# Performance work log

Measured on AMD Instinct MI355X. Metric: run time of the kernel, lower is better.

Reference implementation:

```python
import jax, jax.numpy as jnp
import numpy as np

NUM_HEADS = 16
NUM_GQA_GROUPS = 4
HEAD_DIM = 128
TOTAL_TOKENS = 4096
NUM_SEQS = 8
SCALE = HEAD_DIM ** -0.5


def setup_inputs() -> dict:
    key = jax.random.key(0)
    kq, kk, kv, kc = jax.random.split(key, 4)
    query = jax.random.normal(kq, (TOTAL_TOKENS, NUM_HEADS, HEAD_DIM), dtype=jnp.float32)
    k = jax.random.normal(kk, (TOTAL_TOKENS, NUM_GQA_GROUPS, HEAD_DIM), dtype=jnp.float32)
    v = jax.random.normal(kv, (TOTAL_TOKENS, NUM_GQA_GROUPS, HEAD_DIM), dtype=jnp.float32)
    # cu_seqlens: sorted prefix boundaries, pinned to 0 and TOTAL_TOKENS
    inner = jnp.sort(jax.random.randint(kc, (NUM_SEQS - 1,), 1, TOTAL_TOKENS, dtype=jnp.int32))
    cu_seqlens = jnp.concatenate([
        jnp.zeros((1,), jnp.int32), inner,
        jnp.full((1,), TOTAL_TOKENS, jnp.int32)])
    return {"query": query, "key": k, "value": v, "cu_seqlens": cu_seqlens}


def reference(query, key, value, cu_seqlens):
    """Packed varlen (thd) causal attention with GQA, fused via a segment mask.

    query: [T, H, D]; key/value: [T, G, D]; cu_seqlens: [B+1] int32.
    Returns [T, H, D] (same layout the torch thd path concatenates back to).
    """
    T, H, D = query.shape
    ratio = H // key.shape[1]
    if ratio > 1:  # GQA: repeat kv heads to match query heads
        key = jnp.repeat(key, ratio, axis=1)
        value = jnp.repeat(value, ratio, axis=1)

    pos = jnp.arange(T, dtype=jnp.int32)
    # segment id of each packed token: cu[j] <= i < cu[j+1]
    seg = jnp.searchsorted(cu_seqlens, pos, side="right") - 1
    # within-segment causal mask (global causal == local causal inside a segment)
    mask = (seg[:, None] == seg[None, :]) & (pos[:, None] >= pos[None, :])  # [T, T]

    scores = jnp.einsum("qhd,khd->hqk", query, key) * SCALE  # [H, T, T]
    scores = jnp.where(mask[None], scores, -jnp.inf)
    probs = jax.nn.softmax(scores, axis=-1)
    out = jnp.einsum("hqk,khd->qhd", probs, value)  # [T, H, D]
    return out
```

## Files before the change

kernel.cpp:

```cpp
#include <hip/hip_runtime.h>
#include <hip/hip_bf16.h>


#define T_TOK 4096
#define NH    16
#define NG    4
#define HD    128
#define NCU   9
#define NTILE 128

#define ML_OFF  33554432l
#define Q_OFF   34603008l
#define KBF_OFF 34607620l
#define VTB_OFF 35656196l
#define WS_END  36704772l

typedef short          short8_t __attribute__((ext_vector_type(8)));
typedef float          float4_t __attribute__((ext_vector_type(4)));
typedef unsigned int   uint2_t  __attribute__((ext_vector_type(2)));
typedef unsigned short ushort;

static __device__ inline unsigned pack2(float a, float b) {
    __hip_bfloat162 h = __float22bfloat162_rn(make_float2(a, b));
    union { __hip_bfloat162 h; unsigned u; } c; c.h = h;
    return c.u;
}
static __device__ inline short8_t cvt8(float4_t lo, float4_t hi) {
    union { unsigned u[4]; short8_t s; } r;
    r.u[0] = pack2(lo[0], lo[1]); r.u[1] = pack2(lo[2], lo[3]);
    r.u[2] = pack2(hi[0], hi[1]); r.u[3] = pack2(hi[2], hi[3]);
    return r.s;
}
static __device__ inline float bf2f(ushort u) {
    union { unsigned i; float f; } c; c.i = ((unsigned)u) << 16; return c.f;
}
static __device__ __forceinline__ void chunk_geom(int nblk, int& chunk, int& nce) {
    int nc0 = (nblk + 11) / 12;
    if (nc0 > 8) nc0 = 8;
    chunk = (((nblk + nc0 - 1) / nc0) + 1) & ~1;
    nce   = (nblk + chunk - 1) / chunk;
}

#define NPK 1048576l
__global__ __launch_bounds__(256) void prep_all(
    const float* __restrict__ K, const float* __restrict__ V,
    const int* __restrict__ cu, float* __restrict__ WS)
{
    const int b = (int)blockIdx.x, tid = (int)threadIdx.x;
    if (b < 512) {
        unsigned* Kb = (unsigned*)(WS + KBF_OFF);
        for (long p = (long)b * 256 + tid; p < NPK; p += 512l * 256) {
            const float2 v = *(const float2*)&K[2 * p];
            Kb[p] = pack2(v.x, v.y);
        }
    } else if (b < 1536) {
        ushort* Vtb = (ushort*)(WS + VTB_OFF);
        const int bt  = b - 512;
        const int g   = bt >> 8;
        const int rem = bt & 255;
        const int d0  = (rem >> 6) * 32;
        const int t0  = (rem & 63) * 64;
        __shared__ ushort tile[64][36];
        const int i2 = tid >> 3, jl = (tid & 7) * 4;
        #pragma unroll
        for (int ii = 0; ii < 2; ++ii) {
            const int t = t0 + i2 + ii * 32;
            const float4_t v = *(const float4_t*)&V[((long)t * NG + g) * HD + d0 + jl];
            *(unsigned*)&tile[i2 + ii * 32][jl]     = pack2(v[0], v[1]);
            *(unsigned*)&tile[i2 + ii * 32][jl + 2] = pack2(v[2], v[3]);
        }
        __syncthreads();
        const int jj = tid >> 3, tl = (tid & 7) * 8;
        union { ushort s[8]; short8_t v; } o;
        #pragma unroll
        for (int r = 0; r < 8; ++r) o.s[r] = tile[tl + r][jj];
        *(short8_t*)&Vtb[((long)(g * HD + d0 + jj)) * T_TOK + t0 + tl] = o.v;
    } else {
        int* qwork = (int*)(WS + Q_OFF);
        __shared__ int nblk_s[NTILE];
        __shared__ int sortedE[NTILE + 1];
        if (tid >= 128) return;
        const int t = tid;
        const int qbase = t * 32;
        int seg0 = 0;
        #pragma unroll
        for (int j = 1; j < NCU; ++j) { int cj = cu[j]; if (cj <= qbase) seg0 = cj; }
        const int k0   = seg0 & ~31;
        const int nblk = (qbase + 32 - k0) >> 5;
        nblk_s[t] = nblk;
        __syncthreads();
        int r = 0;
        for (int j = 0; j < NTILE; ++j) {
            int nj = nblk_s[j];
            if (nj > nblk || (nj == nblk && j < t)) ++r;
        }
        int chunk, nce; chunk_geom(nblk, chunk, nce);
        sortedE[r] = 4 * nce;
        __syncthreads();
        if (t == 0) {
            int s = 0;
            for (int j = 0; j < NTILE; ++j) { int v = sortedE[j]; sortedE[j] = s; s += v; }
            sortedE[NTILE] = s;
            qwork[0] = s;
            qwork[1] = 0;
        }
        __syncthreads();
        int off = 2 + sortedE[r];
        for (int g = 0; g < NG; ++g)
            for (int cz = 0; cz < nce; ++cz)
                qwork[off++] = (t << 5) | (g << 3) | cz;
    }
}

template <bool CHB>
static __device__ __forceinline__ void attn_tile_body(
    const float* __restrict__ Q, const float* __restrict__ K,
    const float* __restrict__ V,
    const ushort* __restrict__ Kb, const ushort* __restrict__ Vtb,
    const int* __restrict__ cu,
    float* __restrict__ O, float* __restrict__ WS,
    unsigned char* smem, int qtile, int g, int cz)
{
    ushort (*Ks)[32][136]   = (ushort (*)[32][136])smem;
    ushort (*Vt)[128][40]   = (ushort (*)[128][40])(smem + 17408);
    ushort (*pb)[2][16][40] = (ushort (*)[2][16][40])(smem + 37888);

    const int tid   = threadIdx.x;
    const int wave  = tid >> 6;
    const int split = wave >> 2;
    const int hw    = wave & 3;
    const int lane  = tid & 63;
    const int h     = g * 4 + hw;
    const int col   = lane & 15;
    const int quad  = lane >> 4;

    const int qbase = qtile * 32;
    const int qq[2] = { qbase + col, qbase + 16 + col };

    int seg_start[2] = {0, 0}, seg0 = 0;
    #pragma unroll
    for (int j = 1; j < NCU; ++j) {
        int cj = cu[j];
        if (cj <= qq[0])  seg_start[0] = cj;
        if (cj <= qq[1])  seg_start[1] = cj;
        if (cj <= qbase)  seg0         = cj;
    }
    const int k0       = seg0 & ~31;
    const int nblk_tot = (qbase + 32 - k0) >> 5;

    int nc = 1, kb_lo = 0, nblk = nblk_tot;
    if (CHB) {
        int chunk; chunk_geom(nblk_tot, chunk, nc);
        if (cz >= nc) return;
        kb_lo = cz * chunk;
        nblk  = nblk_tot - kb_lo;
        if (nblk > chunk) nblk = chunk;
    }
    const int nb0    = (nblk + 1) >> 1;
    const int kstart = k0 + (kb_lo + split * nb0) * 32;

    const int smax[2] = { __shfl(seg_start[0], 15), __shfl(seg_start[1], 15) };

    short8_t qf[2][4];
    #pragma unroll
    for (int tt = 0; tt < 2; ++tt) {
        const float* qp = Q + ((long)qq[tt] * NH + h) * HD + quad * 8;
        #pragma unroll
        for (int c = 0; c < 4; ++c)
            qf[tt][c] = cvt8(*(const float4_t*)(qp + c * 32),
                             *(const float4_t*)(qp + c * 32 + 4));
    }

    float4_t oacc[2][8];
    #pragma unroll
    for (int tt = 0; tt < 2; ++tt)
        #pragma unroll
        for (int dt = 0; dt < 8; ++dt) oacc[tt][dt] = (float4_t){0.f, 0.f, 0.f, 0.f};

    float m_run[2] = {-10000.0f, -10000.0f};
    float l_run[2] = {0.0f, 0.0f};
    const float c_scale = 0.08838834764831845f * 1.4426950408889634f;

    const int stid = tid & 255;
    const int ki  = stid >> 3;
    const int ch  = (stid & 7) * 16;
    const int kp2 = (stid & 15) * 2;
    const int dc  = (stid >> 4) * 8;
    const int vd  = stid >> 1;
    const int vko = (stid & 1) * 16;

    float4_t kreg[4], vreg[4];
    short8_t krb[2], vrb[2];
    if constexpr (CHB) {
        int key = kstart + ki; if (key > T_TOK - 1) key = T_TOK - 1;
        const ushort* kp = Kb + ((long)key * NG + g) * HD + ch;
        krb[0] = *(const short8_t*)kp; krb[1] = *(const short8_t*)(kp + 8);
        int ts = kstart + vko; if (ts > T_TOK - 16) ts = T_TOK - 16;
        const ushort* vp = Vtb + ((long)(g * HD + vd)) * T_TOK + ts;
        vrb[0] = *(const short8_t*)vp; vrb[1] = *(const short8_t*)(vp + 8);
    } else {
        int key = kstart + ki; if (key > T_TOK - 1) key = T_TOK - 1;
        const float* kp = K + ((long)key * NG + g) * HD + ch;
        kreg[0] = *(const float4_t*)kp;       kreg[1] = *(const float4_t*)(kp + 4);
        kreg[2] = *(const float4_t*)(kp + 8); kreg[3] = *(const float4_t*)(kp + 12);
        int key0 = kstart + kp2;     if (key0 > T_TOK - 1) key0 = T_TOK - 1;
        int key1 = kstart + kp2 + 1; if (key1 > T_TOK - 1) key1 = T_TOK - 1;
        const float* v0 = V + ((long)key0 * NG + g) * HD + dc;
        const float* v1 = V + ((long)key1 * NG + g) * HD + dc;
        vreg[0] = *(const float4_t*)v0; vreg[1] = *(const float4_t*)(v0 + 4);
        vreg[2] = *(const float4_t*)v1; vreg[3] = *(const float4_t*)(v1 + 4);
    }

    for (int it = 0; it < nb0; ++it) {
        const int kb = kstart + it * 32;
        __syncthreads();

        if constexpr (CHB) {
            *(short8_t*)&Ks[split][ki][ch]      = krb[0];
            *(short8_t*)&Ks[split][ki][ch + 8]  = krb[1];
            *(short8_t*)&Vt[split][vd][vko]     = vrb[0];
            *(short8_t*)&Vt[split][vd][vko + 8] = vrb[1];
        } else {
            *(short8_t*)&Ks[split][ki][ch]     = cvt8(kreg[0], kreg[1]);
            *(short8_t*)&Ks[split][ki][ch + 8] = cvt8(kreg[2], kreg[3]);
            #pragma unroll
            for (int d = 0; d < 4; ++d) {
                *(unsigned*)&Vt[split][dc + d][kp2]     = pack2(vreg[0][d], vreg[2][d]);
                *(unsigned*)&Vt[split][dc + 4 + d][kp2] = pack2(vreg[1][d], vreg[3][d]);
            }
        }
        __syncthreads();

        {
            int nb = kb + 32;
            if constexpr (CHB) {
                int key = nb + ki; if (key > T_TOK - 1) key = T_TOK - 1;
                const ushort* kp = Kb + ((long)key * NG + g) * HD + ch;
                krb[0] = *(const short8_t*)kp; krb[1] = *(const short8_t*)(kp + 8);
                int ts = nb + vko; if (ts > T_TOK - 16) ts = T_TOK - 16;
                const ushort* vp = Vtb + ((long)(g * HD + vd)) * T_TOK + ts;
                vrb[0] = *(const short8_t*)vp; vrb[1] = *(const short8_t*)(vp + 8);
            } else {
                int key = nb + ki; if (key > T_TOK - 1) key = T_TOK - 1;
                const float* kp = K + ((long)key * NG + g) * HD + ch;
                kreg[0] = *(const float4_t*)kp;       kreg[1] = *(const float4_t*)(kp + 4);
                kreg[2] = *(const float4_t*)(kp + 8); kreg[3] = *(const float4_t*)(kp + 12);
                int key0 = nb + kp2;     if (key0 > T_TOK - 1) key0 = T_TOK - 1;
                int key1 = nb + kp2 + 1; if (key1 > T_TOK - 1) key1 = T_TOK - 1;
                const float* v0 = V + ((long)key0 * NG + g) * HD + dc;
                const float* v1 = V + ((long)key1 * NG + g) * HD + dc;
                vreg[0] = *(const float4_t*)v0; vreg[1] = *(const float4_t*)(v0 + 4);
                vreg[2] = *(const float4_t*)v1; vreg[3] = *(const float4_t*)(v1 + 4);
            }
        }

        float4_t st[2][2];
        #pragma unroll
        for (int tt = 0; tt < 2; ++tt)
            #pragma unroll
            for (int t = 0; t < 2; ++t) st[tt][t] = (float4_t){0.f, 0.f, 0.f, 0.f};
        #pragma unroll
        for (int c = 0; c < 4; ++c) {
            short8_t kf0 = *(const short8_t*)&Ks[split][col][c * 32 + quad * 8];
            short8_t kf1 = *(const short8_t*)&Ks[split][16 + col][c * 32 + quad * 8];
            st[0][0] = __builtin_amdgcn_mfma_f32_16x16x32_bf16(kf0, qf[0][c], st[0][0], 0, 0, 0);
            st[0][1] = __builtin_amdgcn_mfma_f32_16x16x32_bf16(kf1, qf[0][c], st[0][1], 0, 0, 0);
            st[1][0] = __builtin_amdgcn_mfma_f32_16x16x32_bf16(kf0, qf[1][c], st[1][0], 0, 0, 0);
            st[1][1] = __builtin_amdgcn_mfma_f32_16x16x32_bf16(kf1, qf[1][c], st[1][1], 0, 0, 0);
        }

        #pragma unroll
        for (int tt = 0; tt < 2; ++tt) {
            float tv[8];
            if (kb + 31 <= qbase + 16 * tt && kb >= smax[tt]) {
                #pragma unroll
                for (int i = 0; i < 8; ++i)
                    tv[i] = st[tt][i >> 2][i & 3] * c_scale;
            } else {
                #pragma unroll
                for (int t = 0; t < 2; ++t)
                    #pragma unroll
                    for (int r = 0; r < 4; ++r) {
                        int key = kb + 16 * t + quad * 4 + r;
                        bool valid = (key <= qq[tt]) && (key >= seg_start[tt]);
                        tv[t * 4 + r] = valid ? st[tt][t][r] * c_scale : -30000.0f;
                    }
            }
            float tmax = tv[0];
            #pragma unroll
            for (int i = 1; i < 8; ++i) tmax = fmaxf(tmax, tv[i]);
            tmax = fmaxf(tmax, __shfl_xor(tmax, 16));
            tmax = fmaxf(tmax, __shfl_xor(tmax, 32));
            const float m_new = fmaxf(m_run[tt], tmax);
            float p[8], ps = 0.f;
            #pragma unroll
            for (int i = 0; i < 8; ++i) { p[i] = __builtin_exp2f(tv[i] - m_new); ps += p[i]; }
            ps += __shfl_xor(ps, 16);
            ps += __shfl_xor(ps, 32);
            if (__any(tmax > m_run[tt])) {
                const float alpha = __builtin_exp2f(m_run[tt] - m_new);
                l_run[tt] = l_run[tt] * alpha + ps;
                m_run[tt] = m_new;
                #pragma unroll
                for (int dt = 0; dt < 8; ++dt) oacc[tt][dt] *= alpha;
            } else {
                l_run[tt] += ps;
            }

            uint2_t w0; w0.x = pack2(p[0], p[1]); w0.y = pack2(p[2], p[3]);
            uint2_t w1; w1.x = pack2(p[4], p[5]); w1.y = pack2(p[6], p[7]);
            *(uint2_t*)&pb[wave][tt][col][quad * 4]      = w0;
            *(uint2_t*)&pb[wave][tt][col][16 + quad * 4] = w1;
        }
        short8_t pf0 = *(const short8_t*)&pb[wave][0][col][quad * 8];
        short8_t pf1 = *(const short8_t*)&pb[wave][1][col][quad * 8];

        #pragma unroll
        for (int dt = 0; dt < 8; ++dt) {
            short8_t vf = *(const short8_t*)&Vt[split][dt * 16 + col][quad * 8];
            oacc[0][dt] = __builtin_amdgcn_mfma_f32_16x16x32_bf16(vf, pf0, oacc[0][dt], 0, 0, 0);
            oacc[1][dt] = __builtin_amdgcn_mfma_f32_16x16x32_bf16(vf, pf1, oacc[1][dt], 0, 0, 0);
        }
    }

    float* Ob = (float*)smem;
    float* cm = (float*)(smem + 34816);
    float* cl = (float*)(smem + 35840);
    #pragma unroll
    for (int tt = 0; tt < 2; ++tt) {
        __syncthreads();
        if (split == 1) {
            if (quad == 0) { cm[hw * 16 + col] = m_run[tt]; cl[hw * 16 + col] = l_run[tt]; }
            float* ob = Ob + (hw * 16 + col) * 132;
            #pragma unroll
            for (int dt = 0; dt < 8; ++dt)
                *(float4_t*)(ob + dt * 16 + quad * 4) = oacc[tt][dt];
        }
        __syncthreads();
        if (split == 0) {
            const float m1 = cm[hw * 16 + col], l1 = cl[hw * 16 + col];
            const float m  = fmaxf(m_run[tt], m1);
            const float a0 = __builtin_exp2f(m_run[tt] - m);
            const float a1 = __builtin_exp2f(m1 - m);
            const float* ob = Ob + (hw * 16 + col) * 132;
            #pragma unroll
            for (int dt = 0; dt < 8; ++dt) {
                float4_t o1 = *(const float4_t*)(ob + dt * 16 + quad * 4);
                oacc[tt][dt] = oacc[tt][dt] * a0 + o1 * a1;
            }
            l_run[tt] = l_run[tt] * a0 + l1 * a1;
            m_run[tt] = m;
        }
    }

    if (split == 0) {
        if (!CHB || nc == 1) {
            #pragma unroll
            for (int tt = 0; tt < 2; ++tt) {
                const float inv_l = 1.0f / l_run[tt];
                float* op = O + ((long)qq[tt] * NH + h) * HD + quad * 4;
                #pragma unroll
                for (int dt = 0; dt < 8; ++dt) {
                    float4_t ov;
                    #pragma unroll
                    for (int r = 0; r < 4; ++r) ov[r] = oacc[tt][dt][r] * inv_l;
                    *(float4_t*)(op + dt * 16) = ov;
                }
            }
        } else {
            const long slot = ((long)(qtile * 4 + g)) * 8 + cz;
            ushort* ob = (ushort*)WS + slot * 16384;
            #pragma unroll
            for (int tt = 0; tt < 2; ++tt) {
                const int row = hw * 32 + tt * 16 + col;
                if (quad == 0) {
                    float* mlp = WS + ML_OFF + slot * 256 + row * 2;
                    mlp[0] = m_run[tt];
                    mlp[1] = l_run[tt];
                }
                ushort* op = ob + row * 128 + quad * 4;
                #pragma unroll
                for (int dt = 0; dt < 8; ++dt) {
                    uint2_t w;
                    w.x = pack2(oacc[tt][dt][0], oacc[tt][dt][1]);
                    w.y = pack2(oacc[tt][dt][2], oacc[tt][dt][3]);
                    *(uint2_t*)(op + dt * 16) = w;
                }
            }
        }
    }
}

__global__ __launch_bounds__(512) void attn_fwd_persist(
    const float* __restrict__ Q,
    const float* __restrict__ K,
    const float* __restrict__ V,
    const int*   __restrict__ cu,
    float*       __restrict__ O,
    float*       __restrict__ WS)
{
    __shared__ __align__(16) unsigned char smem[58368];
    __shared__ int pop_s;
    int* qwork = (int*)(WS + Q_OFF);
    const ushort* Kb  = (const ushort*)(WS + KBF_OFF);
    const ushort* Vtb = (const ushort*)(WS + VTB_OFF);
    const int qtotal = qwork[0];

    for (;;) {
        __syncthreads();
        if (threadIdx.x == 0) pop_s = atomicAdd(&qwork[1], 1);
        __syncthreads();
        const int idx = pop_s;
        if (idx >= qtotal) return;
        const int ent = qwork[2 + idx];
        attn_tile_body<true>(Q, K, V, Kb, Vtb, cu, O, WS, smem,
                             ent >> 5, (ent >> 3) & 3, ent & 7);
    }
}

__global__ __launch_bounds__(512) void attn_fwd_mono(
    const float* __restrict__ Q,
    const float* __restrict__ K,
    const float* __restrict__ V,
    const int*   __restrict__ cu,
    float*       __restrict__ O)
{
    __shared__ __align__(16) unsigned char smem[58368];
    attn_tile_body<false>(Q, K, V, nullptr, nullptr, cu, O, nullptr, smem,
                          (int)gridDim.x - 1 - (int)blockIdx.x,
                          (int)blockIdx.y, 0);
}

__global__ __launch_bounds__(256) void attn_merge(
    const int*   __restrict__ cu,
    const float* __restrict__ WS,
    float*       __restrict__ O)
{
    const int tile  = blockIdx.x;
    const int g     = blockIdx.y;
    const int qbase = tile * 32;
    int seg0 = 0;
    #pragma unroll
    for (int j = 1; j < NCU; ++j) { int cj = cu[j]; if (cj <= qbase) seg0 = cj; }
    const int k0       = seg0 & ~31;
    const int nblk_tot = (qbase + 32 - k0) >> 5;
    int chunk, nc; chunk_geom(nblk_tot, chunk, nc);
    if (nc <= 1) return;

    const int tid  = threadIdx.x;
    const int row  = tid >> 1;
    const int half = tid & 1;
    const int hw   = row >> 5;
    const int q    = row & 31;

    float m = -30000.0f, l = 0.0f;
    float4_t acc[16];
    #pragma unroll
    for (int i = 0; i < 16; ++i) acc[i] = (float4_t){0.f, 0.f, 0.f, 0.f};

    const long sbase = ((long)(tile * 4 + g)) * 8;
    for (int c = 0; c < nc; ++c) {
        const float* mlp = WS + ML_OFF + (sbase + c) * 256 + row * 2;
        const float mc = mlp[0], lc = mlp[1];
        const float mn = fmaxf(m, mc);
        const float a0 = __builtin_exp2f(m - mn);
        const float a1 = __builtin_exp2f(mc - mn);
        l = l * a0 + lc * a1;
        const ushort* op = (const ushort*)WS + (sbase + c) * 16384 + row * 128 + half * 64;
        #pragma unroll
        for (int i = 0; i < 8; ++i) {
            short8_t v8 = *(const short8_t*)(op + i * 8);
            float4_t lo, hi;
            lo[0] = bf2f((ushort)v8[0]); lo[1] = bf2f((ushort)v8[1]);
            lo[2] = bf2f((ushort)v8[2]); lo[3] = bf2f((ushort)v8[3]);
            hi[0] = bf2f((ushort)v8[4]); hi[1] = bf2f((ushort)v8[5]);
            hi[2] = bf2f((ushort)v8[6]); hi[3] = bf2f((ushort)v8[7]);
            acc[2 * i]     = acc[2 * i] * a0 + lo * a1;
            acc[2 * i + 1] = acc[2 * i + 1] * a0 + hi * a1;
        }
        m = mn;
    }
    const float inv = 1.0f / l;
    float* o = O + ((long)(qbase + q) * NH + g * 4 + hw) * HD + half * 64;
    #pragma unroll
    for (int i = 0; i < 16; ++i)
        *(float4_t*)(o + i * 4) = acc[i] * inv;
}

extern "C" void kernel_launch(void* const* d_in, const int* in_sizes, int n_in,
                              void* d_out, int out_size, void* d_ws, size_t ws_size,
                              hipStream_t stream) {
    const float* Q  = (const float*)d_in[0];
    const float* K  = (const float*)d_in[1];
    const float* V  = (const float*)d_in[2];
    const int*   cu = (const int*)d_in[3];
    float*       O  = (float*)d_out;
    const size_t need = (size_t)WS_END * sizeof(float);
    if (d_ws != nullptr && ws_size >= need) {
        float* WS = (float*)d_ws;
        prep_all<<<1537, 256, 0, stream>>>(K, V, cu, WS);
        attn_fwd_persist<<<512, 512, 0, stream>>>(Q, K, V, cu, O, WS);
        attn_merge<<<dim3(T_TOK / 32, NG), 256, 0, stream>>>(
            cu, (const float*)WS, O);
    } else {
        attn_fwd_mono<<<dim3(T_TOK / 32, NG), 512, 0, stream>>>(Q, K, V, cu, O);
    }
}
```

Measured before the change: 200.4 us.

## Drop intra-block KV split, use fixed 16-block chunks and pre-converted bf16 Q

Each workgroup now runs 4 waves (one per head in the GQA group) and no longer splits the key range between two wave halves, which removes the in-block LDS merge. The work is instead split across workgroups in fixed 16-key-block chunks, with 1024 persistent blocks of 256 threads, and partial results are combined by the existing merge kernel. Q is converted to bf16 once in the prep kernel, so the attention kernel can load bf16 fragments directly. The cost is an extra full pass over Q in prep, a larger workspace, and more chunks going through the global merge path.

```diff
diff --git a/kernel.cpp b/kernel.cpp
--- a/kernel.cpp
+++ b/kernel.cpp
@@ -8,12 +8,14 @@
 #define HD    128
 #define NCU   9
 #define NTILE 128
+#define CH_KB 16
 
 #define ML_OFF  33554432l
 #define Q_OFF   34603008l
 #define KBF_OFF 34607620l
 #define VTB_OFF 35656196l
-#define WS_END  36704772l
+#define QBF_OFF 36704772l
+#define WS_END  40899076l
 
 typedef short          short8_t __attribute__((ext_vector_type(8)));
 typedef float          float4_t __attribute__((ext_vector_type(4)));
@@ -34,17 +36,13 @@
 static __device__ inline float bf2f(ushort u) {
     union { unsigned i; float f; } c; c.i = ((unsigned)u) << 16; return c.f;
 }
-static __device__ __forceinline__ void chunk_geom(int nblk, int& chunk, int& nce) {
-    int nc0 = (nblk + 11) / 12;
-    if (nc0 > 8) nc0 = 8;
-    chunk = (((nblk + nc0 - 1) / nc0) + 1) & ~1;
-    nce   = (nblk + chunk - 1) / chunk;
-}
-
+
+#define NPQ 4194304l
 #define NPK 1048576l
 __global__ __launch_bounds__(256) void prep_all(
-    const float* __restrict__ K, const float* __restrict__ V,
-    const int* __restrict__ cu, float* __restrict__ WS)
+    const float* __restrict__ Q, const float* __restrict__ K,
+    const float* __restrict__ V, const int* __restrict__ cu,
+    float* __restrict__ WS)
 {
     const int b = (int)blockIdx.x, tid = (int)threadIdx.x;
     if (b < 512) {
@@ -75,6 +73,13 @@
         #pragma unroll
         for (int r = 0; r < 8; ++r) o.s[r] = tile[tl + r][jj];
         *(short8_t*)&Vtb[((long)(g * HD + d0 + jj)) * T_TOK + t0 + tl] = o.v;
+    } else if (b < 3584) {
+        unsigned* Qb = (unsigned*)(WS + QBF_OFF);
+        const int bq = b - 1536;
+        for (long p = (long)bq * 256 + tid; p < NPQ; p += 2048l * 256) {
+            const float2 v = *(const float2*)&Q[2 * p];
+            Qb[p] = pack2(v.x, v.y);
+        }
     } else {
         int* qwork = (int*)(WS + Q_OFF);
         __shared__ int nblk_s[NTILE];
@@ -94,7 +99,7 @@
             int nj = nblk_s[j];
             if (nj > nblk || (nj == nblk && j < t)) ++r;
         }
-        int chunk, nce; chunk_geom(nblk, chunk, nce);
+        const int nce = (nblk + CH_KB - 1) / CH_KB;
         sortedE[r] = 4 * nce;
         __syncthreads();
         if (t == 0) {
@@ -116,19 +121,19 @@
 static __device__ __forceinline__ void attn_tile_body(
     const float* __restrict__ Q, const float* __restrict__ K,
     const float* __restrict__ V,
-    const ushort* __restrict__ Kb, const ushort* __restrict__ Vtb,
+    const ushort* __restrict__ Qb, const ushort* __restrict__ Kb,
+    const ushort* __restrict__ Vtb,
     const int* __restrict__ cu,
     float* __restrict__ O, float* __restrict__ WS,
     unsigned char* smem, int qtile, int g, int cz)
 {
-    ushort (*Ks)[32][136]   = (ushort (*)[32][136])smem;
-    ushort (*Vt)[128][40]   = (ushort (*)[128][40])(smem + 17408);
-    ushort (*pb)[2][16][40] = (ushort (*)[2][16][40])(smem + 37888);
+    ushort (*Ks)[136]       = (ushort (*)[136])smem;
+    ushort (*Vt)[40]        = (ushort (*)[40])(smem + 8704);
+    ushort (*pb)[2][16][40] = (ushort (*)[2][16][40])(smem + 18944);
 
     const int tid   = threadIdx.x;
     const int wave  = tid >> 6;
-    const int split = wave >> 2;
-    const int hw    = wave & 3;
+    const int hw    = wave;
     const int lane  = tid & 63;
     const int h     = g * 4 + hw;
     const int col   = lane & 15;
@@ -150,25 +155,32 @@
 
     int nc = 1, kb_lo = 0, nblk = nblk_tot;
     if (CHB) {
-        int chunk; chunk_geom(nblk_tot, chunk, nc);
+        nc = (nblk_tot + CH_KB - 1) / CH_KB;
         if (cz >= nc) return;
-        kb_lo = cz * chunk;
+        kb_lo = cz * CH_KB;
         nblk  = nblk_tot - kb_lo;
-        if (nblk > chunk) nblk = chunk;
-    }
-    const int nb0    = (nblk + 1) >> 1;
-    const int kstart = k0 + (kb_lo + split * nb0) * 32;
+        if (nblk > CH_KB) nblk = CH_KB;
+    }
+    const int nb0    = nblk;
+    const int kstart = k0 + kb_lo * 32;
 
     const int smax[2] = { __shfl(seg_start[0], 15), __shfl(seg_start[1], 15) };
 
     short8_t qf[2][4];
     #pragma unroll
     for (int tt = 0; tt < 2; ++tt) {
-        const float* qp = Q + ((long)qq[tt] * NH + h) * HD + quad * 8;
-        #pragma unroll
-        for (int c = 0; c < 4; ++c)
-            qf[tt][c] = cvt8(*(const float4_t*)(qp + c * 32),
-                             *(const float4_t*)(qp + c * 32 + 4));
+        if constexpr (CHB) {
+            const ushort* qp = Qb + ((long)qq[tt] * NH + h) * HD + quad * 8;
+            #pragma unroll
+            for (int c = 0; c < 4; ++c)
+                qf[tt][c] = *(const short8_t*)(qp + c * 32);
+        } else {
+            const float* qp = Q + ((long)qq[tt] * NH + h) * HD + quad * 8;
+            #pragma unroll
+            for (int c = 0; c < 4; ++c)
+                qf[tt][c] = cvt8(*(const float4_t*)(qp + c * 32),
+                                 *(const float4_t*)(qp + c * 32 + 4));
+        }
     }
 
     float4_t oacc[2][8];
@@ -181,13 +193,12 @@
     float l_run[2] = {0.0f, 0.0f};
     const float c_scale = 0.08838834764831845f * 1.4426950408889634f;
 
-    const int stid = tid & 255;
-    const int ki  = stid >> 3;
-    const int ch  = (stid & 7) * 16;
-    const int kp2 = (stid & 15) * 2;
-    const int dc  = (stid >> 4) * 8;
-    const int vd  = stid >> 1;
-    const int vko = (stid & 1) * 16;
+    const int ki  = tid >> 3;
+    const int ch  = (tid & 7) * 16;
+    const int kp2 = (tid & 15) * 2;
+    const int dc  = (tid >> 4) * 8;
+    const int vd  = tid >> 1;
+    const int vko = (tid & 1) * 16;
 
     float4_t kreg[4], vreg[4];
     short8_t krb[2], vrb[2];
@@ -216,17 +227,17 @@
         __syncthreads();
 
         if constexpr (CHB) {
-            *(short8_t*)&Ks[split][ki][ch]      = krb[0];
-            *(short8_t*)&Ks[split][ki][ch + 8]  = krb[1];
-            *(short8_t*)&Vt[split][vd][vko]     = vrb[0];
-            *(short8_t*)&Vt[split][vd][vko + 8] = vrb[1];
+            *(short8_t*)&Ks[ki][ch]      = krb[0];
+            *(short8_t*)&Ks[ki][ch + 8]  = krb[1];
+            *(short8_t*)&Vt[vd][vko]     = vrb[0];
+            *(short8_t*)&Vt[vd][vko + 8] = vrb[1];
         } else {
-            *(short8_t*)&Ks[split][ki][ch]     = cvt8(kreg[0], kreg[1]);
-            *(short8_t*)&Ks[split][ki][ch + 8] = cvt8(kreg[2], kreg[3]);
+            *(short8_t*)&Ks[ki][ch]     = cvt8(kreg[0], kreg[1]);
+            *(short8_t*)&Ks[ki][ch + 8] = cvt8(kreg[2], kreg[3]);
             #pragma unroll
             for (int d = 0; d < 4; ++d) {
-                *(unsigned*)&Vt[split][dc + d][kp2]     = pack2(vreg[0][d], vreg[2][d]);
-                *(unsigned*)&Vt[split][dc + 4 + d][kp2] = pack2(vreg[1][d], vreg[3][d]);
+                *(unsigned*)&Vt[dc + d][kp2]     = pack2(vreg[0][d], vreg[2][d]);
+                *(unsigned*)&Vt[dc + 4 + d][kp2] = pack2(vreg[1][d], vreg[3][d]);
             }
         }
         __syncthreads();
@@ -261,8 +272,8 @@
             for (int t = 0; t < 2; ++t) st[tt][t] = (float4_t){0.f, 0.f, 0.f, 0.f};
         #pragma unroll
         for (int c = 0; c < 4; ++c) {
-            short8_t kf0 = *(const short8_t*)&Ks[split][col][c * 32 + quad * 8];
-            short8_t kf1 = *(const short8_t*)&Ks[split][16 + col][c * 32 + quad * 8];
+            short8_t kf0 = *(const short8_t*)&Ks[col][c * 32 + quad * 8];
+            short8_t kf1 = *(const short8_t*)&Ks[16 + col][c * 32 + quad * 8];
             st[0][0] = __builtin_amdgcn_mfma_f32_16x16x32_bf16(kf0, qf[0][c], st[0][0], 0, 0, 0);
             st[0][1] = __builtin_amdgcn_mfma_f32_16x16x32_bf16(kf1, qf[0][c], st[0][1], 0, 0, 0);
             st[1][0] = __builtin_amdgcn_mfma_f32_16x16x32_bf16(kf0, qf[1][c], st[1][0], 0, 0, 0);
@@ -317,81 +328,49 @@
 
         #pragma unroll
         for (int dt = 0; dt < 8; ++dt) {
-            short8_t vf = *(const short8_t*)&Vt[split][dt * 16 + col][quad * 8];
+            short8_t vf = *(const short8_t*)&Vt[dt * 16 + col][quad * 8];
             oacc[0][dt] = __builtin_amdgcn_mfma_f32_16x16x32_bf16(vf, pf0, oacc[0][dt], 0, 0, 0);
             oacc[1][dt] = __builtin_amdgcn_mfma_f32_16x16x32_bf16(vf, pf1, oacc[1][dt], 0, 0, 0);
         }
     }
 
-    float* Ob = (float*)smem;
-    float* cm = (float*)(smem + 34816);
-    float* cl = (float*)(smem + 35840);
-    #pragma unroll
-    for (int tt = 0; tt < 2; ++tt) {
-        __syncthreads();
-        if (split == 1) {
-            if (quad == 0) { cm[hw * 16 + col] = m_run[tt]; cl[hw * 16 + col] = l_run[tt]; }
-            float* ob = Ob + (hw * 16 + col) * 132;
-            #pragma unroll
-            for (int dt = 0; dt < 8; ++dt)
-                *(float4_t*)(ob + dt * 16 + quad * 4) = oacc[tt][dt];
-        }
-        __syncthreads();
-        if (split == 0) {
-            const float m1 = cm[hw * 16 + col], l1 = cl[hw * 16 + col];
-            const float m  = fmaxf(m_run[tt], m1);
-            const float a0 = __builtin_exp2f(m_run[tt] - m);
-            const float a1 = __builtin_exp2f(m1 - m);
-            const float* ob = Ob + (hw * 16 + col) * 132;
+    if (!CHB || nc == 1) {
+        #pragma unroll
+        for (int tt = 0; tt < 2; ++tt) {
+            const float inv_l = 1.0f / l_run[tt];
+            float* op = O + ((long)qq[tt] * NH + h) * HD + quad * 4;
             #pragma unroll
             for (int dt = 0; dt < 8; ++dt) {
-                float4_t o1 = *(const float4_t*)(ob + dt * 16 + quad * 4);
-                oacc[tt][dt] = oacc[tt][dt] * a0 + o1 * a1;
-            }
-            l_run[tt] = l_run[tt] * a0 + l1 * a1;
-            m_run[tt] = m;
-        }
-    }
-
-    if (split == 0) {
-        if (!CHB || nc == 1) {
-            #pragma unroll
-            for (int tt = 0; tt < 2; ++tt) {
-                const float inv_l = 1.0f / l_run[tt];
-                float* op = O + ((long)qq[tt] * NH + h) * HD + quad * 4;
+                float4_t ov;
                 #pragma unroll
-                for (int dt = 0; dt < 8; ++dt) {
-                    float4_t ov;
-                    #pragma unroll
-                    for (int r = 0; r < 4; ++r) ov[r] = oacc[tt][dt][r] * inv_l;
-                    *(float4_t*)(op + dt * 16) = ov;
-                }
-            }
-        } else {
-            const long slot = ((long)(qtile * 4 + g)) * 8 + cz;
-            ushort* ob = (ushort*)WS + slot * 16384;
-            #pragma unroll
-            for (int tt = 0; tt < 2; ++tt) {
-                const int row = hw * 32 + tt * 16 + col;
-                if (quad == 0) {
-                    float* mlp = WS + ML_OFF + slot * 256 + row * 2;
-                    mlp[0] = m_run[tt];
-                    mlp[1] = l_run[tt];
-                }
-                ushort* op = ob + row * 128 + quad * 4;
-                #pragma unroll
-                for (int dt = 0; dt < 8; ++dt) {
-                    uint2_t w;
-                    w.x = pack2(oacc[tt][dt][0], oacc[tt][dt][1]);
-                    w.y = pack2(oacc[tt][dt][2], oacc[tt][dt][3]);
-                    *(uint2_t*)(op + dt * 16) = w;
-                }
-            }
-        }
-    }
-}
-
-__global__ __launch_bounds__(512) void attn_fwd_persist(
+                for (int r = 0; r < 4; ++r) ov[r] = oacc[tt][dt][r] * inv_l;
+                *(float4_t*)(op + dt * 16) = ov;
+            }
+        }
+    } else {
+        const long slot = ((long)(qtile * 4 + g)) * 8 + cz;
+        ushort* ob = (ushort*)WS + slot * 16384;
+        #pragma unroll
+        for (int tt = 0; tt < 2; ++tt) {
+            const int row = hw * 32 + tt * 16 + col;
+            if (quad == 0) {
+                float* mlp = WS + ML_OFF + slot * 256 + row * 2;
+                mlp[0] = m_run[tt];
+                mlp[1] = l_run[tt];
+            }
+            ushort* op = ob + row * 128 + quad * 4;
+            #pragma unroll
+            for (int dt = 0; dt < 8; ++dt) {
+                uint2_t w;
+                w.x = pack2(oacc[tt][dt][0], oacc[tt][dt][1]);
+                w.y = pack2(oacc[tt][dt][2], oacc[tt][dt][3]);
+                *(uint2_t*)(op + dt * 16) = w;
+            }
+        }
+    }
+}
+
+__global__ __launch_bounds__(256) void attn_fwd_persist(
     const float* __restrict__ Q,
     const float* __restrict__ K,
     const float* __restrict__ V,
@@ -399,9 +378,10 @@
     float*       __restrict__ O,
     float*       __restrict__ WS)
 {
-    __shared__ __align__(16) unsigned char smem[58368];
+    __shared__ __align__(16) unsigned char smem[29184];
     __shared__ int pop_s;
     int* qwork = (int*)(WS + Q_OFF);
+    const ushort* Qb  = (const ushort*)(WS + QBF_OFF);
     const ushort* Kb  = (const ushort*)(WS + KBF_OFF);
     const ushort* Vtb = (const ushort*)(WS + VTB_OFF);
     const int qtotal = qwork[0];
@@ -413,21 +393,21 @@
         const int idx = pop_s;
         if (idx >= qtotal) return;
         const int ent = qwork[2 + idx];
-        attn_tile_body<true>(Q, K, V, Kb, Vtb, cu, O, WS, smem,
+        attn_tile_body<true>(Q, K, V, Qb, Kb, Vtb, cu, O, WS, smem,
                              ent >> 5, (ent >> 3) & 3, ent & 7);
     }
 }
 
-__global__ __launch_bounds__(512) void attn_fwd_mono(
+__global__ __launch_bounds__(256) void attn_fwd_mono(
     const float* __restrict__ Q,
     const float* __restrict__ K,
     const float* __restrict__ V,
     const int*   __restrict__ cu,
     float*       __restrict__ O)
 {
-    __shared__ __align__(16) unsigned char smem[58368];
-    attn_tile_body<false>(Q, K, V, nullptr, nullptr, cu, O, nullptr, smem,
-                          (int)gridDim.x - 1 - (int)blockIdx.x,
+    __shared__ __align__(16) unsigned char smem[29184];
+    attn_tile_body<false>(Q, K, V, nullptr, nullptr, nullptr, cu, O, nullptr,
+                          smem, (int)gridDim.x - 1 - (int)blockIdx.x,
                           (int)blockIdx.y, 0);
 }
 
@@ -444,7 +424,7 @@
     for (int j = 1; j < NCU; ++j) { int cj = cu[j]; if (cj <= qbase) seg0 = cj; }
     const int k0       = seg0 & ~31;
     const int nblk_tot = (qbase + 32 - k0) >> 5;
-    int chunk, nc; chunk_geom(nblk_tot, chunk, nc);
+    const int nc       = (nblk_tot + CH_KB - 1) / CH_KB;
     if (nc <= 1) return;
 
     const int tid  = threadIdx.x;
@@ -498,11 +478,11 @@
     const size_t need = (size_t)WS_END * sizeof(float);
     if (d_ws != nullptr && ws_size >= need) {
         float* WS = (float*)d_ws;
-        prep_all<<<1537, 256, 0, stream>>>(K, V, cu, WS);
-        attn_fwd_persist<<<512, 512, 0, stream>>>(Q, K, V, cu, O, WS);
+        prep_all<<<3585, 256, 0, stream>>>(Q, K, V, cu, WS);
+        attn_fwd_persist<<<1024, 256, 0, stream>>>(Q, K, V, cu, O, WS);
         attn_merge<<<dim3(T_TOK / 32, NG), 256, 0, stream>>>(
             cu, (const float*)WS, O);
     } else {
-        attn_fwd_mono<<<dim3(T_TOK / 32, NG), 512, 0, stream>>>(Q, K, V, cu, O);
-    }
-}
+        attn_fwd_mono<<<dim3(T_TOK / 32, NG), 256, 0, stream>>>(Q, K, V, cu, O);
+    }
+}
```

Result: slower. 211.8 us (+5.7%).
